# Performance work log

Hardware: AMD Instinct MI355X
Metric: run time of the kernel (lower is better)

Reference implementation:

```python
import jax, jax.numpy as jnp
import numpy as np

# 8-neighborhood order from compute_lbp_batch
_NEIGHBORS = [(-1, -1), (-1, 0), (-1, 1), (0, 1), (1, 1), (1, 0), (1, -1), (0, -1)]


def compute_lbp(images):
    """Vectorized census-transform LBP. images: [B,H,W] -> codes [B,H,W] in [0,255]."""
    B, H, W = images.shape
    padded = jnp.pad(images, ((0, 0), (1, 1), (1, 1)))  # zero pad, matches torch F.pad
    center = images
    code = jnp.zeros((B, H, W), dtype=jnp.float32)
    for bit, (dy, dx) in enumerate(_NEIGHBORS):
        nbr = padded[:, 1 + dy:1 + dy + H, 1 + dx:1 + dx + W]
        code = code + (nbr >= center).astype(jnp.float32) * np.float32(2.0 ** bit)
    return code


def glt_thresholds(latent_thresholds):
    """Cumulative learned thresholds mapped to [-1, 1] (GLTEstimator.forward)."""
    positive = jax.nn.relu(latent_thresholds) + 1e-5
    normalized = positive / positive.sum()
    return jnp.cumsum(normalized) * 2.0 - 1.0


def setup_inputs() -> dict:
    key = jax.random.key(0)
    k1, k2 = jax.random.split(key)
    images = jax.random.uniform(k1, (256, 128, 128), dtype=jnp.float32)
    latent_thresholds = jax.random.uniform(k2, (8,), dtype=jnp.float32)
    return {"images": images, "latent_thresholds": latent_thresholds}


def reference(images, latent_thresholds):
    # 1) LBP census transform -> codes in [0, 255]
    codes = compute_lbp(images)
    # 2) normalize codes to [-1, 1] to match GLT threshold range
    x = codes * np.float32(1.0 / 127.5) - np.float32(1.0)
    # 3) thermometer encoding against cumulative learned thresholds
    thr = glt_thresholds(latent_thresholds)  # [M]
    out = (x[..., None] >= thr).astype(jnp.float32)  # [B,H,W,M]
    return out
```

## Files before the change

kernel.cpp:

```cpp
#include <hip/hip_runtime.h>


#define BN 256
#define HN 128
#define WN 128

typedef float float4v __attribute__((ext_vector_type(4)));

__global__ __launch_bounds__(256) void lbp_glt_kernel(
    const float* __restrict__ img,
    const float* __restrict__ lat,
    float* __restrict__ out)
{
    __shared__ int s_cmin[8];
    const int tid = threadIdx.x;

    if (tid < 8) {
        float pos[8];
        #pragma unroll
        for (int i = 0; i < 8; ++i) {
            float v = lat[i];
            v = v > 0.0f ? v : 0.0f;
            pos[i] = __fadd_rn(v, 1e-5f);
        }
        float total = __fadd_rn(
            __fadd_rn(__fadd_rn(pos[0], pos[1]), __fadd_rn(pos[2], pos[3])),
            __fadd_rn(__fadd_rn(pos[4], pos[5]), __fadd_rn(pos[6], pos[7])));
        float cum = 0.0f;
        for (int i = 0; i <= tid; ++i)
            cum = __fadd_rn(cum, __fdiv_rn(pos[i], total));
        const float thr = __fsub_rn(__fmul_rn(cum, 2.0f), 1.0f);

        const float s = (float)(1.0 / 127.5);
        int g = (int)ceilf((thr + 1.0f) * 127.5f);
        if (g < 0) g = 0;
        if (g > 256) g = 256;
        while (g > 0) {
            float x = __fsub_rn(__fmul_rn((float)(g - 1), s), 1.0f);
            if (x >= thr) --g; else break;
        }
        while (g < 256) {
            float x = __fsub_rn(__fmul_rn((float)g, s), 1.0f);
            if (x < thr) ++g; else break;
        }
        s_cmin[tid] = g;
    }
    __syncthreads();

    const long long c4 = (long long)blockIdx.x * 256 + tid;
    const int half = (int)(c4 & 1);
    const long long p = c4 >> 1;
    const int x = (int)(p & (WN - 1));
    const int y = (int)((p >> 7) & (HN - 1));
    const int b = (int)(p >> 14);

    const float* base = img + ((size_t)b << 14) + ((size_t)y << 7) + x;
    const float c = base[0];

    const bool ym = (y > 0), yp = (y < HN - 1);
    const bool xm = (x > 0), xp = (x < WN - 1);

    const float v_tl = (ym && xm) ? base[-WN - 1] : 0.0f;
    const float v_tc = ym         ? base[-WN]     : 0.0f;
    const float v_tr = (ym && xp) ? base[-WN + 1] : 0.0f;
    const float v_r  = xp         ? base[1]       : 0.0f;
    const float v_br = (yp && xp) ? base[WN + 1]  : 0.0f;
    const float v_bc = yp         ? base[WN]      : 0.0f;
    const float v_bl = (yp && xm) ? base[WN - 1]  : 0.0f;
    const float v_l  = xm         ? base[-1]      : 0.0f;

    const int code = (v_tl >= c ?   1 : 0)
                   | (v_tc >= c ?   2 : 0)
                   | (v_tr >= c ?   4 : 0)
                   | (v_r  >= c ?   8 : 0)
                   | (v_br >= c ?  16 : 0)
                   | (v_bc >= c ?  32 : 0)
                   | (v_bl >= c ?  64 : 0)
                   | (v_l  >= c ? 128 : 0);

    const int t0 = half * 4;
    float4v o;
    o.x = code >= s_cmin[t0 + 0] ? 1.0f : 0.0f;
    o.y = code >= s_cmin[t0 + 1] ? 1.0f : 0.0f;
    o.z = code >= s_cmin[t0 + 2] ? 1.0f : 0.0f;
    o.w = code >= s_cmin[t0 + 3] ? 1.0f : 0.0f;

    float4v* op = (float4v*)out + c4;
    __builtin_nontemporal_store(o, op);
}

extern "C" void kernel_launch(void* const* d_in, const int* in_sizes, int n_in,
                              void* d_out, int out_size, void* d_ws, size_t ws_size,
                              hipStream_t stream) {
    const float* img = (const float*)d_in[0];
    const float* lat = (const float*)d_in[1];
    float* out = (float*)d_out;

    const long long n_chunks = (long long)BN * HN * WN * 2;
    const int blocks = (int)(n_chunks / 256);
    lbp_glt_kernel<<<dim3(blocks), dim3(256), 0, stream>>>(img, lat, out);
}
```

Before: 178.3 us.

## Use persistent grid-stride loop with one pixel per thread and wave shuffles

```diff
diff --git a/kernel.cpp b/kernel.cpp
--- a/kernel.cpp
+++ b/kernel.cpp
@@ -4,6 +4,9 @@
 #define BN 256
 #define HN 128
 #define WN 128
+#define NPIX (BN * HN * WN)
+#define NBLOCKS 2048
+#define NTHREADS (NBLOCKS * 256)
 
 typedef float float4v __attribute__((ext_vector_type(4)));
 
@@ -47,46 +50,65 @@
     }
     __syncthreads();
 
-    const long long c4 = (long long)blockIdx.x * 256 + tid;
-    const int half = (int)(c4 & 1);
-    const long long p = c4 >> 1;
-    const int x = (int)(p & (WN - 1));
-    const int y = (int)((p >> 7) & (HN - 1));
-    const int b = (int)(p >> 14);
+    const int lane = tid & 63;
+    const int h4 = (lane & 1) * 4;
+    const int cm0 = s_cmin[h4 + 0];
+    const int cm1 = s_cmin[h4 + 1];
+    const int cm2 = s_cmin[h4 + 2];
+    const int cm3 = s_cmin[h4 + 3];
 
-    const float* base = img + ((size_t)b << 14) + ((size_t)y << 7) + x;
-    const float c = base[0];
+    const int tg = blockIdx.x * 256 + tid;
+    const int srcA = lane >> 1;
+    const int srcB = 32 + (lane >> 1);
 
-    const bool ym = (y > 0), yp = (y < HN - 1);
-    const bool xm = (x > 0), xp = (x < WN - 1);
+    #pragma unroll 2
+    for (int it = 0; it < NPIX / NTHREADS; ++it) {
+        const int p = it * NTHREADS + tg;
+        const int x = p & (WN - 1);
+        const int y = (p >> 7) & (HN - 1);
 
-    const float v_tl = (ym && xm) ? base[-WN - 1] : 0.0f;
-    const float v_tc = ym         ? base[-WN]     : 0.0f;
-    const float v_tr = (ym && xp) ? base[-WN + 1] : 0.0f;
-    const float v_r  = xp         ? base[1]       : 0.0f;
-    const float v_br = (yp && xp) ? base[WN + 1]  : 0.0f;
-    const float v_bc = yp         ? base[WN]      : 0.0f;
-    const float v_bl = (yp && xm) ? base[WN - 1]  : 0.0f;
-    const float v_l  = xm         ? base[-1]      : 0.0f;
+        const float* base = img + (size_t)p;
+        const float c = base[0];
 
-    const int code = (v_tl >= c ?   1 : 0)
-                   | (v_tc >= c ?   2 : 0)
-                   | (v_tr >= c ?   4 : 0)
-                   | (v_r  >= c ?   8 : 0)
-                   | (v_br >= c ?  16 : 0)
-                   | (v_bc >= c ?  32 : 0)
-                   | (v_bl >= c ?  64 : 0)
-                   | (v_l  >= c ? 128 : 0);
+        const bool ym = (y > 0), yp = (y < HN - 1);
+        const bool xm = (x > 0), xp = (x < WN - 1);
 
-    const int t0 = half * 4;
-    float4v o;
-    o.x = code >= s_cmin[t0 + 0] ? 1.0f : 0.0f;
-    o.y = code >= s_cmin[t0 + 1] ? 1.0f : 0.0f;
-    o.z = code >= s_cmin[t0 + 2] ? 1.0f : 0.0f;
-    o.w = code >= s_cmin[t0 + 3] ? 1.0f : 0.0f;
+        const float v_tl = (ym && xm) ? base[-WN - 1] : 0.0f;
+        const float v_tc = ym         ? base[-WN]     : 0.0f;
+        const float v_tr = (ym && xp) ? base[-WN + 1] : 0.0f;
+        const float v_r  = xp         ? base[1]       : 0.0f;
+        const float v_br = (yp && xp) ? base[WN + 1]  : 0.0f;
+        const float v_bc = yp         ? base[WN]      : 0.0f;
+        const float v_bl = (yp && xm) ? base[WN - 1]  : 0.0f;
+        const float v_l  = xm         ? base[-1]      : 0.0f;
 
-    float4v* op = (float4v*)out + c4;
-    __builtin_nontemporal_store(o, op);
+        const int code = (v_tl >= c ?   1 : 0)
+                       | (v_tc >= c ?   2 : 0)
+                       | (v_tr >= c ?   4 : 0)
+                       | (v_r  >= c ?   8 : 0)
+                       | (v_br >= c ?  16 : 0)
+                       | (v_bc >= c ?  32 : 0)
+                       | (v_bl >= c ?  64 : 0)
+                       | (v_l  >= c ? 128 : 0);
+
+        const int codeA = __shfl(code, srcA, 64);
+        const int codeB = __shfl(code, srcB, 64);
+
+        float4v oA, oB;
+        oA.x = codeA >= cm0 ? 1.0f : 0.0f;
+        oA.y = codeA >= cm1 ? 1.0f : 0.0f;
+        oA.z = codeA >= cm2 ? 1.0f : 0.0f;
+        oA.w = codeA >= cm3 ? 1.0f : 0.0f;
+        oB.x = codeB >= cm0 ? 1.0f : 0.0f;
+        oB.y = codeB >= cm1 ? 1.0f : 0.0f;
+        oB.z = codeB >= cm2 ? 1.0f : 0.0f;
+        oB.w = codeB >= cm3 ? 1.0f : 0.0f;
+
+        const size_t cbase = 2 * (size_t)(p & ~63);
+        float4v* op = (float4v*)out + cbase;
+        op[lane]      = oA;
+        op[64 + lane] = oB;
+    }
 }
 
 extern "C" void kernel_launch(void* const* d_in, const int* in_sizes, int n_in,
@@ -96,7 +118,5 @@
     const float* lat = (const float*)d_in[1];
     float* out = (float*)d_out;
 
-    const long long n_chunks = (long long)BN * HN * WN * 2;
-    const int blocks = (int)(n_chunks / 256);
-    lbp_glt_kernel<<<dim3(blocks), dim3(256), 0, stream>>>(img, lat, out);
+    lbp_glt_kernel<<<dim3(NBLOCKS), dim3(256), 0, stream>>>(img, lat, out);
 }
```

After: 153.8 us, median of 2. 1.16x faster.

## Compute four pixels per thread with vector row loads and lane shuffles

Applied to the files above, without the earlier changes.

```diff
diff --git a/kernel.cpp b/kernel.cpp
--- a/kernel.cpp
+++ b/kernel.cpp
@@ -1,9 +1,8 @@
 #include <hip/hip_runtime.h>
 
 
-#define BN 256
-#define HN 128
 #define WN 128
+#define NROWS (256 * 128)
 
 typedef float float4v __attribute__((ext_vector_type(4)));
 
@@ -47,46 +46,70 @@
     }
     __syncthreads();
 
-    const long long c4 = (long long)blockIdx.x * 256 + tid;
-    const int half = (int)(c4 & 1);
-    const long long p = c4 >> 1;
-    const int x = (int)(p & (WN - 1));
-    const int y = (int)((p >> 7) & (HN - 1));
-    const int b = (int)(p >> 14);
+    int cm[8];
+    #pragma unroll
+    for (int t = 0; t < 8; ++t) cm[t] = __builtin_amdgcn_readfirstlane(s_cmin[t]);
 
-    const float* base = img + ((size_t)b << 14) + ((size_t)y << 7) + x;
-    const float c = base[0];
+    const int lane  = tid & 63;
+    const int gwave = (blockIdx.x << 2) + (tid >> 6);
+    const int row   = (gwave << 1) + (lane >> 5);
+    const int y     = row & (WN - 1);
+    const int xi    = (lane & 31) << 2;
 
-    const bool ym = (y > 0), yp = (y < HN - 1);
-    const bool xm = (x > 0), xp = (x < WN - 1);
+    const float* rowptr = img + ((size_t)row << 7) + xi;
 
-    const float v_tl = (ym && xm) ? base[-WN - 1] : 0.0f;
-    const float v_tc = ym         ? base[-WN]     : 0.0f;
-    const float v_tr = (ym && xp) ? base[-WN + 1] : 0.0f;
-    const float v_r  = xp         ? base[1]       : 0.0f;
-    const float v_br = (yp && xp) ? base[WN + 1]  : 0.0f;
-    const float v_bc = yp         ? base[WN]      : 0.0f;
-    const float v_bl = (yp && xm) ? base[WN - 1]  : 0.0f;
-    const float v_l  = xm         ? base[-1]      : 0.0f;
+    float4v mid = *(const float4v*)rowptr;
+    const bool has_top = (y > 0);
+    const bool has_bot = (y < WN - 1);
+    float4v top = *(const float4v*)(rowptr + (has_top ? -WN : 0));
+    float4v bot = *(const float4v*)(rowptr + (has_bot ?  WN : 0));
+    if (!has_top) top = (float4v){0.0f, 0.0f, 0.0f, 0.0f};
+    if (!has_bot) bot = (float4v){0.0f, 0.0f, 0.0f, 0.0f};
 
-    const int code = (v_tl >= c ?   1 : 0)
-                   | (v_tc >= c ?   2 : 0)
-                   | (v_tr >= c ?   4 : 0)
-                   | (v_r  >= c ?   8 : 0)
-                   | (v_br >= c ?  16 : 0)
-                   | (v_bc >= c ?  32 : 0)
-                   | (v_bl >= c ?  64 : 0)
-                   | (v_l  >= c ? 128 : 0);
+    float lm = __shfl(mid.w, lane - 1, 64);
+    float lt = __shfl(top.w, lane - 1, 64);
+    float lb = __shfl(bot.w, lane - 1, 64);
+    float rm = __shfl(mid.x, lane + 1, 64);
+    float rt = __shfl(top.x, lane + 1, 64);
+    float rb = __shfl(bot.x, lane + 1, 64);
+    const bool xm = (lane & 31) != 0;
+    const bool xp = (lane & 31) != 31;
+    if (!xm) { lm = 0.0f; lt = 0.0f; lb = 0.0f; }
+    if (!xp) { rm = 0.0f; rt = 0.0f; rb = 0.0f; }
 
-    const int t0 = half * 4;
-    float4v o;
-    o.x = code >= s_cmin[t0 + 0] ? 1.0f : 0.0f;
-    o.y = code >= s_cmin[t0 + 1] ? 1.0f : 0.0f;
-    o.z = code >= s_cmin[t0 + 2] ? 1.0f : 0.0f;
-    o.w = code >= s_cmin[t0 + 3] ? 1.0f : 0.0f;
+    const float t6[6] = { lt, top.x, top.y, top.z, top.w, rt };
+    const float m6[6] = { lm, mid.x, mid.y, mid.z, mid.w, rm };
+    const float b6[6] = { lb, bot.x, bot.y, bot.z, bot.w, rb };
 
-    float4v* op = (float4v*)out + c4;
-    __builtin_nontemporal_store(o, op);
+    float4v o[8];
+    #pragma unroll
+    for (int j = 0; j < 4; ++j) {
+        const float c = m6[j + 1];
+        const int code = (t6[j]     >= c ?   1 : 0)
+                       | (t6[j + 1] >= c ?   2 : 0)
+                       | (t6[j + 2] >= c ?   4 : 0)
+                       | (m6[j + 2] >= c ?   8 : 0)
+                       | (b6[j + 2] >= c ?  16 : 0)
+                       | (b6[j + 1] >= c ?  32 : 0)
+                       | (b6[j]     >= c ?  64 : 0)
+                       | (m6[j + 1 - 1] >= c ? 128 : 0);
+        float4v oa, ob;
+        oa.x = code >= cm[0] ? 1.0f : 0.0f;
+        oa.y = code >= cm[1] ? 1.0f : 0.0f;
+        oa.z = code >= cm[2] ? 1.0f : 0.0f;
+        oa.w = code >= cm[3] ? 1.0f : 0.0f;
+        ob.x = code >= cm[4] ? 1.0f : 0.0f;
+        ob.y = code >= cm[5] ? 1.0f : 0.0f;
+        ob.z = code >= cm[6] ? 1.0f : 0.0f;
+        ob.w = code >= cm[7] ? 1.0f : 0.0f;
+        o[2 * j]     = oa;
+        o[2 * j + 1] = ob;
+    }
+
+    const size_t pbase = ((size_t)row << 7) + xi;
+    float4v* op = (float4v*)out + (pbase << 1);
+    #pragma unroll
+    for (int k = 0; k < 8; ++k) op[k] = o[k];
 }
 
 extern "C" void kernel_launch(void* const* d_in, const int* in_sizes, int n_in,
@@ -96,7 +119,5 @@
     const float* lat = (const float*)d_in[1];
     float* out = (float*)d_out;
 
-    const long long n_chunks = (long long)BN * HN * WN * 2;
-    const int blocks = (int)(n_chunks / 256);
-    lbp_glt_kernel<<<dim3(blocks), dim3(256), 0, stream>>>(img, lat, out);
+    lbp_glt_kernel<<<dim3(NROWS / 8), dim3(256), 0, stream>>>(img, lat, out);
 }
```

New measurement: 163.3 us. 1.09x faster.
